# Kernel optimization log

Hardware: AMD Instinct MI355X
Metric: run time of the kernel (lower is better)

The kernel has to match this reference:

```python
import jax, jax.numpy as jnp
import numpy as np

N = 20000        # nodes
E = 320000       # edges (avg degree 16)
IN = 128         # in_channels
D = 64           # out_channels == per-head dim (PyG TransformerConv)
H = 4            # heads
EPS_BN = 1e-5


def setup_inputs() -> dict:
    key = jax.random.key(0)
    ks = jax.random.split(key, 12)
    x = jax.random.normal(ks[0], (N, IN), jnp.float32)
    edge_index = jax.random.randint(ks[1], (2, E), 0, N, dtype=jnp.int64)
    s = 1.0 / np.sqrt(IN)
    Wq = jax.random.normal(ks[2], (IN, H * D), jnp.float32) * s
    bq = jnp.zeros((H * D,), jnp.float32)
    Wk = jax.random.normal(ks[3], (IN, H * D), jnp.float32) * s
    bk = jnp.zeros((H * D,), jnp.float32)
    Wv = jax.random.normal(ks[4], (IN, H * D), jnp.float32) * s
    bv = jnp.zeros((H * D,), jnp.float32)
    Wskip = jax.random.normal(ks[5], (IN, D), jnp.float32) * s
    bskip = jnp.zeros((D,), jnp.float32)
    gamma = jnp.ones((D,), jnp.float32)
    beta = jnp.zeros((D,), jnp.float32)
    return {"x": x, "edge_index": edge_index, "Wq": Wq, "bq": bq,
            "Wk": Wk, "bk": bk, "Wv": Wv, "bv": bv,
            "Wskip": Wskip, "bskip": bskip, "gamma": gamma, "beta": beta}


def reference(x, edge_index, Wq, bq, Wk, bk, Wv, bv, Wskip, bskip, gamma, beta):
    src = edge_index[0]   # message source j
    dst = edge_index[1]   # message target i
    # node-level projections, [N, H, D]
    q = (x @ Wq + bq).reshape(N, H, D)
    k = (x @ Wk + bk).reshape(N, H, D)
    v = (x @ Wv + bv).reshape(N, H, D)
    # per-edge attention logits [E, H]
    scores = jnp.einsum('ehd,ehd->eh', q[dst], k[src]) / jnp.sqrt(jnp.float32(D))
    # segment softmax over incoming edges of each target node
    smax = jax.ops.segment_max(scores, dst, num_segments=N)
    smax = jnp.where(jnp.isfinite(smax), smax, 0.0)  # isolated nodes
    p = jnp.exp(scores - smax[dst])
    denom = jax.ops.segment_sum(p, dst, num_segments=N)
    alpha = p / (denom[dst] + 1e-16)                  # [E, H]
    # scatter-aggregate messages: [N, H, D]
    msg = jax.ops.segment_sum(alpha[:, :, None] * v[src], dst, num_segments=N)
    # concat=False -> mean over heads; root skip connection
    out = msg.mean(axis=1) + x @ Wskip + bskip        # [N, D]
    # BatchNorm1d over nodes (training-mode batch stats, biased var)
    mu = out.mean(axis=0)
    var = out.var(axis=0)
    out = (out - mu) * jax.lax.rsqrt(var + EPS_BN) * gamma + beta
    # exact (erf) GELU, dropout = identity at eval
    return jax.nn.gelu(out, approximate=False)
```

## Files before the change

### kernel.cpp

```cpp
#include <hip/hip_runtime.h>
#include <hip/hip_fp16.h>
#include <math.h>

#define NNODES 20000
#define NEDGES 320000
#define CIN 128
#define DOUT 64
#define NHEAD 4
#define HD 256
#define PROJW 320
#define KVW 512
#define NCOL 832
#define NWAVES (1250 * 13)

typedef __attribute__((ext_vector_type(8))) _Float16 half8;
typedef __attribute__((ext_vector_type(4))) float f32x4;

__global__ __launch_bounds__(256) void prep_kernel(
    const float* __restrict__ x,
    const float* __restrict__ Wq, const float* __restrict__ bq,
    const float* __restrict__ Wk, const float* __restrict__ bk,
    const float* __restrict__ Wv, const float* __restrict__ bv,
    const float* __restrict__ Ws, const float* __restrict__ bs,
    _Float16* __restrict__ xh, _Float16* __restrict__ Wth,
    float* __restrict__ bias832)
{
    int i = blockIdx.x * 256 + threadIdx.x;
    if (i < NNODES * CIN / 8) {
        const float4* xv = reinterpret_cast<const float4*>(x);
        float4 u = xv[2 * i], v = xv[2 * i + 1];
        half8 h = { (_Float16)u.x, (_Float16)u.y, (_Float16)u.z, (_Float16)u.w,
                    (_Float16)v.x, (_Float16)v.y, (_Float16)v.z, (_Float16)v.w };
        *reinterpret_cast<half8*>(xh + (size_t)i * 8) = h;
        return;
    }
    i -= NNODES * CIN / 8;
    if (i < NCOL * CIN) {
        int c = i >> 7, k = i & 127;
        float v;
        if (c < 256)      v = Wq[k * HD + c];
        else if (c < 512) v = Wk[k * HD + (c - 256)];
        else if (c < 768) v = Wv[k * HD + (c - 512)];
        else              v = Ws[k * DOUT + (c - 768)];
        Wth[(size_t)c * CIN + k] = (_Float16)v;
        return;
    }
    i -= NCOL * CIN;
    if (i < NCOL) {
        float v;
        if (i < 256)      v = bq[i];
        else if (i < 512) v = bk[i - 256];
        else if (i < 768) v = bv[i - 512];
        else              v = bs[i - 768];
        bias832[i] = v;
    }
}

__global__ __launch_bounds__(256) void wproj_kernel(
    const _Float16* __restrict__ xh, const _Float16* __restrict__ Wth,
    const float* __restrict__ bias832,
    float* __restrict__ proj, __half* __restrict__ kvh)
{
    const int wv = blockIdx.x * 4 + (threadIdx.x >> 6);
    if (wv >= NWAVES) return;
    const int l = threadIdx.x & 63;
    const int ct = wv / 1250, rt = wv % 1250;
    const int row0 = rt * 16, colb = ct * 64;
    const int lrow = l & 15, lk8 = (l >> 4) * 8;

    const _Float16* xr = xh + (size_t)(row0 + lrow) * CIN + lk8;
    const half8 a0 = *reinterpret_cast<const half8*>(xr);
    const half8 a1 = *reinterpret_cast<const half8*>(xr + 32);
    const half8 a2 = *reinterpret_cast<const half8*>(xr + 64);
    const half8 a3 = *reinterpret_cast<const half8*>(xr + 96);

    f32x4 acc[4];
    #pragma unroll
    for (int cg = 0; cg < 4; ++cg) {
        const _Float16* wr = Wth + (size_t)(colb + cg * 16 + lrow) * CIN + lk8;
        const half8 b0 = *reinterpret_cast<const half8*>(wr);
        const half8 b1 = *reinterpret_cast<const half8*>(wr + 32);
        const half8 b2 = *reinterpret_cast<const half8*>(wr + 64);
        const half8 b3 = *reinterpret_cast<const half8*>(wr + 96);
        f32x4 c = {0.f, 0.f, 0.f, 0.f};
        c = __builtin_amdgcn_mfma_f32_16x16x32_f16(a0, b0, c, 0, 0, 0);
        c = __builtin_amdgcn_mfma_f32_16x16x32_f16(a1, b1, c, 0, 0, 0);
        c = __builtin_amdgcn_mfma_f32_16x16x32_f16(a2, b2, c, 0, 0, 0);
        c = __builtin_amdgcn_mfma_f32_16x16x32_f16(a3, b3, c, 0, 0, 0);
        acc[cg] = c;
    }

    const int orow = row0 + (l >> 4) * 4;
    #pragma unroll
    for (int cg = 0; cg < 4; ++cg) {
        const int c = colb + cg * 16 + lrow;
        const float bias = bias832[c];
        if (ct < 4) {
            #pragma unroll
            for (int r = 0; r < 4; ++r)
                proj[(size_t)(orow + r) * PROJW + c] = acc[cg][r] + bias;
        } else if (ct < 12) {
            #pragma unroll
            for (int r = 0; r < 4; ++r)
                kvh[(size_t)(orow + r) * KVW + (c - 256)] = __float2half(acc[cg][r] + bias);
        } else {
            #pragma unroll
            for (int r = 0; r < 4; ++r)
                proj[(size_t)(orow + r) * PROJW + (c - 512)] = acc[cg][r] + bias;
        }
    }
}

__global__ void hist_kernel(const int* __restrict__ ei, int* __restrict__ deg)
{
    int e = blockIdx.x * blockDim.x + threadIdx.x;
    if (e >= NEDGES) return;
    atomicAdd(&deg[ei[NEDGES + e]], 1);
}

__global__ __launch_bounds__(1024) void scan_kernel(
    const int* __restrict__ deg, int* __restrict__ rowptr, int* __restrict__ cursor)
{
    __shared__ int sd[1024];
    const int t = threadIdx.x;
    const int chunk = 20;
    const int base = t * chunk;
    int tsum = 0;
    for (int i = 0; i < chunk; ++i) {
        int idx = base + i;
        tsum += (idx < NNODES) ? deg[idx] : 0;
    }
    sd[t] = tsum; __syncthreads();
    for (int off = 1; off < 1024; off <<= 1) {
        int v = (t >= off) ? sd[t - off] : 0;
        __syncthreads();
        sd[t] += v;
        __syncthreads();
    }
    int run = sd[t] - tsum;
    for (int i = 0; i < chunk; ++i) {
        int idx = base + i;
        if (idx < NNODES) {
            int d = deg[idx];
            rowptr[idx] = run; cursor[idx] = run;
            run += d;
        }
    }
    if (t == 1023) rowptr[NNODES] = sd[1023];
}

__global__ void scatter_kernel(const int* __restrict__ ei, int* __restrict__ cursor,
                               int* __restrict__ col)
{
    int e = blockIdx.x * blockDim.x + threadIdx.x;
    if (e >= NEDGES) return;
    int src = ei[e];
    int dst = ei[NEDGES + e];
    int pos = atomicAdd(&cursor[dst], 1);
    col[pos] = src;
}

__global__ __launch_bounds__(256) void attn_kernel(
    const float* __restrict__ proj, const __half* __restrict__ kvh,
    const int* __restrict__ rowptr, const int* __restrict__ col,
    float* __restrict__ out_pre)
{
    const int node = blockIdx.x * 4 + (threadIdx.x >> 6);
    if (node >= NNODES) return;
    const int lane = threadIdx.x & 63;
    const int lane4 = lane * 4;

    const float4 q = *reinterpret_cast<const float4*>(proj + (size_t)node * PROJW + lane4);

    float m = -INFINITY, l = 0.f;
    float ax = 0.f, ay = 0.f, az = 0.f, aw = 0.f;
    int p = rowptr[node];
    const int pend = rowptr[node + 1];

    int j = (p < pend) ? col[p] : 0;
    const __half* bj = kvh + (size_t)j * KVW + lane4;
    uint2 kraw = *reinterpret_cast<const uint2*>(bj);
    uint2 vraw = *reinterpret_cast<const uint2*>(bj + 256);

    for (; p < pend; ++p) {
        const int p1 = p + 1;
        const int jn = (p1 < pend) ? col[p1] : j;
        const __half* bn = kvh + (size_t)jn * KVW + lane4;
        const uint2 krawn = *reinterpret_cast<const uint2*>(bn);
        const uint2 vrawn = *reinterpret_cast<const uint2*>(bn + 256);

        const float2 k0 = __half22float2(*reinterpret_cast<const __half2*>(&kraw.x));
        const float2 k1 = __half22float2(*reinterpret_cast<const __half2*>(&kraw.y));
        float partial = q.x * k0.x + q.y * k0.y + q.z * k1.x + q.w * k1.y;
        partial += __shfl_xor(partial, 1, 16);
        partial += __shfl_xor(partial, 2, 16);
        partial += __shfl_xor(partial, 4, 16);
        partial += __shfl_xor(partial, 8, 16);
        const float s = partial * 0.125f;
        const float mnew = fmaxf(m, s);
        const float scale = __expf(m - mnew);
        const float pc = __expf(s - mnew);
        const float2 v0 = __half22float2(*reinterpret_cast<const __half2*>(&vraw.x));
        const float2 v1 = __half22float2(*reinterpret_cast<const __half2*>(&vraw.y));
        l = l * scale + pc;
        ax = ax * scale + pc * v0.x;
        ay = ay * scale + pc * v0.y;
        az = az * scale + pc * v1.x;
        aw = aw * scale + pc * v1.y;
        m = mnew;
        kraw = krawn; vraw = vrawn;
    }
    const float inv = 1.f / (l + 1e-16f);
    float rx = ax * inv, ry = ay * inv, rz = az * inv, rw = aw * inv;
    rx += __shfl_xor(rx, 16); rx += __shfl_xor(rx, 32);
    ry += __shfl_xor(ry, 16); ry += __shfl_xor(ry, 32);
    rz += __shfl_xor(rz, 16); rz += __shfl_xor(rz, 32);
    rw += __shfl_xor(rw, 16); rw += __shfl_xor(rw, 32);
    if (lane < 16) {
        const float4 sk = *reinterpret_cast<const float4*>(proj + (size_t)node * PROJW + 256 + lane4);
        float4 o;
        o.x = rx * 0.25f + sk.x;
        o.y = ry * 0.25f + sk.y;
        o.z = rz * 0.25f + sk.z;
        o.w = rw * 0.25f + sk.w;
        *reinterpret_cast<float4*>(out_pre + (size_t)node * DOUT + lane4) = o;
    }
}

__global__ __launch_bounds__(256) void bnred_kernel(
    const float* __restrict__ out_pre, float* __restrict__ bnacc)
{
    const int tid = threadIdx.x;
    const int c = tid & 63, g = tid >> 6;
    float s = 0.f, ss = 0.f;
    for (int r = blockIdx.x * 4 + g; r < NNODES; r += gridDim.x * 4) {
        float v = out_pre[(size_t)r * DOUT + c];
        s += v; ss += v * v;
    }
    __shared__ float sd[256];
    sd[tid] = s; __syncthreads();
    float s4 = 0.f;
    if (g == 0) s4 = sd[tid] + sd[tid + 64] + sd[tid + 128] + sd[tid + 192];
    __syncthreads();
    sd[tid] = ss; __syncthreads();
    if (g == 0) {
        float ss4 = sd[tid] + sd[tid + 64] + sd[tid + 128] + sd[tid + 192];
        atomicAdd(&bnacc[c], s4);
        atomicAdd(&bnacc[64 + c], ss4);
    }
}

__global__ __launch_bounds__(256) void final_kernel(
    const float* __restrict__ out_pre, const float* __restrict__ bnacc,
    const float* __restrict__ gamma, const float* __restrict__ beta,
    float* __restrict__ out)
{
    int idx = blockIdx.x * blockDim.x + threadIdx.x;
    if (idx >= NNODES * DOUT) return;
    const int c = idx & 63;
    const float mu = bnacc[c] * (1.f / NNODES);
    const float var = bnacc[64 + c] * (1.f / NNODES) - mu * mu;
    float v = (out_pre[idx] - mu) * rsqrtf(var + 1e-5f) * gamma[c] + beta[c];
    out[idx] = v * 0.5f * (1.f + erff(v * 0.70710678118654752f));
}

extern "C" void kernel_launch(void* const* d_in, const int* in_sizes, int n_in,
                              void* d_out, int out_size, void* d_ws, size_t ws_size,
                              hipStream_t stream) {
    const float* x     = (const float*)d_in[0];
    const int*   ei    = (const int*)d_in[1];
    const float* Wq    = (const float*)d_in[2];
    const float* bq    = (const float*)d_in[3];
    const float* Wk    = (const float*)d_in[4];
    const float* bk    = (const float*)d_in[5];
    const float* Wv    = (const float*)d_in[6];
    const float* bv    = (const float*)d_in[7];
    const float* Wskip = (const float*)d_in[8];
    const float* bskip = (const float*)d_in[9];
    const float* gamma = (const float*)d_in[10];
    const float* beta  = (const float*)d_in[11];
    float* out = (float*)d_out;

    __half*   kvh    = (__half*)d_ws;
    _Float16* xh     = (_Float16*)((char*)d_ws + 20480000);
    _Float16* Wth    = xh + (size_t)NNODES * CIN;
    float*    bias832= (float*)(Wth + (size_t)NCOL * CIN);
    float*    proj   = bias832 + NCOL;
    float*    out_pre= proj + (size_t)NNODES * PROJW;
    float*    bnacc  = out_pre + (size_t)NNODES * DOUT;
    int*      deg    = (int*)(bnacc + 128);
    int*      rowptr = deg + NNODES;
    int*      cursor = rowptr + NNODES + 1;
    int*      col    = cursor + NNODES;

    hipMemsetAsync(bnacc, 0, (128 + NNODES) * sizeof(int), stream);

    const int prep_total = NNODES * CIN / 8 + NCOL * CIN + NCOL;
    prep_kernel<<<(prep_total + 255) / 256, 256, 0, stream>>>(
        x, Wq, bq, Wk, bk, Wv, bv, Wskip, bskip, xh, Wth, bias832);
    wproj_kernel<<<(NWAVES + 3) / 4, 256, 0, stream>>>(xh, Wth, bias832, proj, kvh);
    hist_kernel<<<(NEDGES + 255) / 256, 256, 0, stream>>>(ei, deg);
    scan_kernel<<<1, 1024, 0, stream>>>(deg, rowptr, cursor);
    scatter_kernel<<<(NEDGES + 255) / 256, 256, 0, stream>>>(ei, cursor, col);
    attn_kernel<<<NNODES / 4, 256, 0, stream>>>(proj, kvh, rowptr, col, out_pre);
    bnred_kernel<<<128, 256, 0, stream>>>(out_pre, bnacc);
    final_kernel<<<(NNODES * DOUT + 255) / 256, 256, 0, stream>>>(
        out_pre, bnacc, gamma, beta, out);
}
```

Before: 264.6 us.

## Fuse graph build into projection kernels and BN reduction into attention

Merges the degree histogram into the prep kernel and the CSR scatter into the projection GEMM kernel as extra independent blocks. It also folds the BatchNorm sum and sum-of-squares reduction into the attention kernel, which now processes two nodes per wave and accumulates per-block partials before the atomics. This cuts the launch count from eight to five and removes the separate pass that re-read out_pre. In exchange it adds more global atomics on bnacc, one pair per block, and mixes heterogeneous work inside single launches.

```diff
diff --git a/kernel.cpp b/kernel.cpp
--- a/kernel.cpp
+++ b/kernel.cpp
@@ -12,18 +12,22 @@
 #define KVW 512
 #define NCOL 832
 #define NWAVES (1250 * 13)
+#define WPROJ_BLOCKS ((NWAVES + 3) / 4)
+#define SCATTER_BLOCKS ((NEDGES + 255) / 256)
+#define PREP_TOTAL (NNODES * CIN / 8 + NCOL * CIN + NCOL)
 
 typedef __attribute__((ext_vector_type(8))) _Float16 half8;
 typedef __attribute__((ext_vector_type(4))) float f32x4;
 
-__global__ __launch_bounds__(256) void prep_kernel(
+__global__ __launch_bounds__(256) void prep_hist_kernel(
     const float* __restrict__ x,
     const float* __restrict__ Wq, const float* __restrict__ bq,
     const float* __restrict__ Wk, const float* __restrict__ bk,
     const float* __restrict__ Wv, const float* __restrict__ bv,
     const float* __restrict__ Ws, const float* __restrict__ bs,
     _Float16* __restrict__ xh, _Float16* __restrict__ Wth,
-    float* __restrict__ bias832)
+    float* __restrict__ bias832,
+    const int* __restrict__ ei, int* __restrict__ deg)
 {
     int i = blockIdx.x * 256 + threadIdx.x;
     if (i < NNODES * CIN / 8) {
@@ -53,14 +57,60 @@
         else if (i < 768) v = bv[i - 512];
         else              v = bs[i - 768];
         bias832[i] = v;
-    }
-}
-
-__global__ __launch_bounds__(256) void wproj_kernel(
+        return;
+    }
+    i -= NCOL;
+    if (i < NEDGES)
+        atomicAdd(&deg[ei[NEDGES + i]], 1);
+}
+
+__global__ __launch_bounds__(1024) void scan_kernel(
+    const int* __restrict__ deg, int* __restrict__ rowptr, int* __restrict__ cursor)
+{
+    __shared__ int sd[1024];
+    const int t = threadIdx.x;
+    const int chunk = 20;
+    const int base = t * chunk;
+    int tsum = 0;
+    for (int i = 0; i < chunk; ++i) {
+        int idx = base + i;
+        tsum += (idx < NNODES) ? deg[idx] : 0;
+    }
+    sd[t] = tsum; __syncthreads();
+    for (int off = 1; off < 1024; off <<= 1) {
+        int v = (t >= off) ? sd[t - off] : 0;
+        __syncthreads();
+        sd[t] += v;
+        __syncthreads();
+    }
+    int run = sd[t] - tsum;
+    for (int i = 0; i < chunk; ++i) {
+        int idx = base + i;
+        if (idx < NNODES) {
+            int d = deg[idx];
+            rowptr[idx] = run; cursor[idx] = run;
+            run += d;
+        }
+    }
+    if (t == 1023) rowptr[NNODES] = sd[1023];
+}
+
+__global__ __launch_bounds__(256) void wproj_scatter_kernel(
     const _Float16* __restrict__ xh, const _Float16* __restrict__ Wth,
     const float* __restrict__ bias832,
-    float* __restrict__ proj, __half* __restrict__ kvh)
-{
+    float* __restrict__ proj, __half* __restrict__ kvh,
+    const int* __restrict__ ei, int* __restrict__ cursor, int* __restrict__ col)
+{
+    if (blockIdx.x >= WPROJ_BLOCKS) {
+        int e = (blockIdx.x - WPROJ_BLOCKS) * 256 + threadIdx.x;
+        if (e < NEDGES) {
+            int src = ei[e];
+            int dst = ei[NEDGES + e];
+            int pos = atomicAdd(&cursor[dst], 1);
+            col[pos] = src;
+        }
+        return;
+    }
     const int wv = blockIdx.x * 4 + (threadIdx.x >> 6);
     if (wv >= NWAVES) return;
     const int l = threadIdx.x & 63;
@@ -111,142 +161,94 @@
     }
 }
 
-__global__ void hist_kernel(const int* __restrict__ ei, int* __restrict__ deg)
-{
-    int e = blockIdx.x * blockDim.x + threadIdx.x;
-    if (e >= NEDGES) return;
-    atomicAdd(&deg[ei[NEDGES + e]], 1);
-}
-
-__global__ __launch_bounds__(1024) void scan_kernel(
-    const int* __restrict__ deg, int* __restrict__ rowptr, int* __restrict__ cursor)
-{
-    __shared__ int sd[1024];
-    const int t = threadIdx.x;
-    const int chunk = 20;
-    const int base = t * chunk;
-    int tsum = 0;
-    for (int i = 0; i < chunk; ++i) {
-        int idx = base + i;
-        tsum += (idx < NNODES) ? deg[idx] : 0;
-    }
-    sd[t] = tsum; __syncthreads();
-    for (int off = 1; off < 1024; off <<= 1) {
-        int v = (t >= off) ? sd[t - off] : 0;
-        __syncthreads();
-        sd[t] += v;
-        __syncthreads();
-    }
-    int run = sd[t] - tsum;
-    for (int i = 0; i < chunk; ++i) {
-        int idx = base + i;
-        if (idx < NNODES) {
-            int d = deg[idx];
-            rowptr[idx] = run; cursor[idx] = run;
-            run += d;
-        }
-    }
-    if (t == 1023) rowptr[NNODES] = sd[1023];
-}
-
-__global__ void scatter_kernel(const int* __restrict__ ei, int* __restrict__ cursor,
-                               int* __restrict__ col)
-{
-    int e = blockIdx.x * blockDim.x + threadIdx.x;
-    if (e >= NEDGES) return;
-    int src = ei[e];
-    int dst = ei[NEDGES + e];
-    int pos = atomicAdd(&cursor[dst], 1);
-    col[pos] = src;
-}
-
-__global__ __launch_bounds__(256) void attn_kernel(
+__global__ __launch_bounds__(256) void attn_bn_kernel(
     const float* __restrict__ proj, const __half* __restrict__ kvh,
     const int* __restrict__ rowptr, const int* __restrict__ col,
-    float* __restrict__ out_pre)
-{
-    const int node = blockIdx.x * 4 + (threadIdx.x >> 6);
-    if (node >= NNODES) return;
+    float* __restrict__ out_pre, float* __restrict__ bnacc)
+{
+    const int wave = threadIdx.x >> 6;
     const int lane = threadIdx.x & 63;
     const int lane4 = lane * 4;
-
-    const float4 q = *reinterpret_cast<const float4*>(proj + (size_t)node * PROJW + lane4);
-
-    float m = -INFINITY, l = 0.f;
-    float ax = 0.f, ay = 0.f, az = 0.f, aw = 0.f;
-    int p = rowptr[node];
-    const int pend = rowptr[node + 1];
-
-    int j = (p < pend) ? col[p] : 0;
-    const __half* bj = kvh + (size_t)j * KVW + lane4;
-    uint2 kraw = *reinterpret_cast<const uint2*>(bj);
-    uint2 vraw = *reinterpret_cast<const uint2*>(bj + 256);
-
-    for (; p < pend; ++p) {
-        const int p1 = p + 1;
-        const int jn = (p1 < pend) ? col[p1] : j;
-        const __half* bn = kvh + (size_t)jn * KVW + lane4;
-        const uint2 krawn = *reinterpret_cast<const uint2*>(bn);
-        const uint2 vrawn = *reinterpret_cast<const uint2*>(bn + 256);
-
-        const float2 k0 = __half22float2(*reinterpret_cast<const __half2*>(&kraw.x));
-        const float2 k1 = __half22float2(*reinterpret_cast<const __half2*>(&kraw.y));
-        float partial = q.x * k0.x + q.y * k0.y + q.z * k1.x + q.w * k1.y;
-        partial += __shfl_xor(partial, 1, 16);
-        partial += __shfl_xor(partial, 2, 16);
-        partial += __shfl_xor(partial, 4, 16);
-        partial += __shfl_xor(partial, 8, 16);
-        const float s = partial * 0.125f;
-        const float mnew = fmaxf(m, s);
-        const float scale = __expf(m - mnew);
-        const float pc = __expf(s - mnew);
-        const float2 v0 = __half22float2(*reinterpret_cast<const __half2*>(&vraw.x));
-        const float2 v1 = __half22float2(*reinterpret_cast<const __half2*>(&vraw.y));
-        l = l * scale + pc;
-        ax = ax * scale + pc * v0.x;
-        ay = ay * scale + pc * v0.y;
-        az = az * scale + pc * v1.x;
-        aw = aw * scale + pc * v1.y;
-        m = mnew;
-        kraw = krawn; vraw = vrawn;
-    }
-    const float inv = 1.f / (l + 1e-16f);
-    float rx = ax * inv, ry = ay * inv, rz = az * inv, rw = aw * inv;
-    rx += __shfl_xor(rx, 16); rx += __shfl_xor(rx, 32);
-    ry += __shfl_xor(ry, 16); ry += __shfl_xor(ry, 32);
-    rz += __shfl_xor(rz, 16); rz += __shfl_xor(rz, 32);
-    rw += __shfl_xor(rw, 16); rw += __shfl_xor(rw, 32);
+    float4 bsum  = make_float4(0.f, 0.f, 0.f, 0.f);
+    float4 bsum2 = make_float4(0.f, 0.f, 0.f, 0.f);
+
+    #pragma unroll
+    for (int t = 0; t < 2; ++t) {
+        const int node = blockIdx.x * 8 + wave * 2 + t;
+
+        const float4 q = *reinterpret_cast<const float4*>(proj + (size_t)node * PROJW + lane4);
+        float m = -INFINITY, l = 0.f;
+        float ax = 0.f, ay = 0.f, az = 0.f, aw = 0.f;
+        int p = rowptr[node];
+        const int pend = rowptr[node + 1];
+
+        int j = (p < pend) ? col[p] : 0;
+        const __half* bj = kvh + (size_t)j * KVW + lane4;
+        uint2 kraw = *reinterpret_cast<const uint2*>(bj);
+        uint2 vraw = *reinterpret_cast<const uint2*>(bj + 256);
+
+        for (; p < pend; ++p) {
+            const int p1 = p + 1;
+            const int jn = (p1 < pend) ? col[p1] : j;
+            const __half* bn = kvh + (size_t)jn * KVW + lane4;
+            const uint2 krawn = *reinterpret_cast<const uint2*>(bn);
+            const uint2 vrawn = *reinterpret_cast<const uint2*>(bn + 256);
+
+            const float2 k0 = __half22float2(*reinterpret_cast<const __half2*>(&kraw.x));
+            const float2 k1 = __half22float2(*reinterpret_cast<const __half2*>(&kraw.y));
+            float partial = q.x * k0.x + q.y * k0.y + q.z * k1.x + q.w * k1.y;
+            partial += __shfl_xor(partial, 1, 16);
+            partial += __shfl_xor(partial, 2, 16);
+            partial += __shfl_xor(partial, 4, 16);
+            partial += __shfl_xor(partial, 8, 16);
+            const float s = partial * 0.125f;
+            const float mnew = fmaxf(m, s);
+            const float scale = __expf(m - mnew);
+            const float pc = __expf(s - mnew);
+            const float2 v0 = __half22float2(*reinterpret_cast<const __half2*>(&vraw.x));
+            const float2 v1 = __half22float2(*reinterpret_cast<const __half2*>(&vraw.y));
+            l = l * scale + pc;
+            ax = ax * scale + pc * v0.x;
+            ay = ay * scale + pc * v0.y;
+            az = az * scale + pc * v1.x;
+            aw = aw * scale + pc * v1.y;
+            m = mnew;
+            kraw = krawn; vraw = vrawn;
+        }
+        const float inv = 1.f / (l + 1e-16f);
+        float rx = ax * inv, ry = ay * inv, rz = az * inv, rw = aw * inv;
+        rx += __shfl_xor(rx, 16); rx += __shfl_xor(rx, 32);
+        ry += __shfl_xor(ry, 16); ry += __shfl_xor(ry, 32);
+        rz += __shfl_xor(rz, 16); rz += __shfl_xor(rz, 32);
+        rw += __shfl_xor(rw, 16); rw += __shfl_xor(rw, 32);
+        if (lane < 16) {
+            const float4 sk = *reinterpret_cast<const float4*>(proj + (size_t)node * PROJW + 256 + lane4);
+            float4 o;
+            o.x = rx * 0.25f + sk.x;
+            o.y = ry * 0.25f + sk.y;
+            o.z = rz * 0.25f + sk.z;
+            o.w = rw * 0.25f + sk.w;
+            *reinterpret_cast<float4*>(out_pre + (size_t)node * DOUT + lane4) = o;
+            bsum.x += o.x; bsum.y += o.y; bsum.z += o.z; bsum.w += o.w;
+            bsum2.x += o.x * o.x; bsum2.y += o.y * o.y;
+            bsum2.z += o.z * o.z; bsum2.w += o.w * o.w;
+        }
+    }
+
+    __shared__ float sred[2][4][64];
     if (lane < 16) {
-        const float4 sk = *reinterpret_cast<const float4*>(proj + (size_t)node * PROJW + 256 + lane4);
-        float4 o;
-        o.x = rx * 0.25f + sk.x;
-        o.y = ry * 0.25f + sk.y;
-        o.z = rz * 0.25f + sk.z;
-        o.w = rw * 0.25f + sk.w;
-        *reinterpret_cast<float4*>(out_pre + (size_t)node * DOUT + lane4) = o;
-    }
-}
-
-__global__ __launch_bounds__(256) void bnred_kernel(
-    const float* __restrict__ out_pre, float* __restrict__ bnacc)
-{
-    const int tid = threadIdx.x;
-    const int c = tid & 63, g = tid >> 6;
-    float s = 0.f, ss = 0.f;
-    for (int r = blockIdx.x * 4 + g; r < NNODES; r += gridDim.x * 4) {
-        float v = out_pre[(size_t)r * DOUT + c];
-        s += v; ss += v * v;
-    }
-    __shared__ float sd[256];
-    sd[tid] = s; __syncthreads();
-    float s4 = 0.f;
-    if (g == 0) s4 = sd[tid] + sd[tid + 64] + sd[tid + 128] + sd[tid + 192];
+        sred[0][wave][lane4 + 0] = bsum.x;  sred[0][wave][lane4 + 1] = bsum.y;
+        sred[0][wave][lane4 + 2] = bsum.z;  sred[0][wave][lane4 + 3] = bsum.w;
+        sred[1][wave][lane4 + 0] = bsum2.x; sred[1][wave][lane4 + 1] = bsum2.y;
+        sred[1][wave][lane4 + 2] = bsum2.z; sred[1][wave][lane4 + 3] = bsum2.w;
+    }
     __syncthreads();
-    sd[tid] = ss; __syncthreads();
-    if (g == 0) {
-        float ss4 = sd[tid] + sd[tid + 64] + sd[tid + 128] + sd[tid + 192];
-        atomicAdd(&bnacc[c], s4);
-        atomicAdd(&bnacc[64 + c], ss4);
+    if (threadIdx.x < 64) {
+        const int c = threadIdx.x;
+        float s  = sred[0][0][c] + sred[0][1][c] + sred[0][2][c] + sred[0][3][c];
+        float ss = sred[1][0][c] + sred[1][1][c] + sred[1][2][c] + sred[1][3][c];
+        atomicAdd(&bnacc[c], s);
+        atomicAdd(&bnacc[64 + c], ss);
     }
 }
 
@@ -295,15 +297,13 @@
 
     hipMemsetAsync(bnacc, 0, (128 + NNODES) * sizeof(int), stream);
 
-    const int prep_total = NNODES * CIN / 8 + NCOL * CIN + NCOL;
-    prep_kernel<<<(prep_total + 255) / 256, 256, 0, stream>>>(
-        x, Wq, bq, Wk, bk, Wv, bv, Wskip, bskip, xh, Wth, bias832);
-    wproj_kernel<<<(NWAVES + 3) / 4, 256, 0, stream>>>(xh, Wth, bias832, proj, kvh);
-    hist_kernel<<<(NEDGES + 255) / 256, 256, 0, stream>>>(ei, deg);
+    const int ph_total = PREP_TOTAL + NEDGES;
+    prep_hist_kernel<<<(ph_total + 255) / 256, 256, 0, stream>>>(
+        x, Wq, bq, Wk, bk, Wv, bv, Wskip, bskip, xh, Wth, bias832, ei, deg);
     scan_kernel<<<1, 1024, 0, stream>>>(deg, rowptr, cursor);
-    scatter_kernel<<<(NEDGES + 255) / 256, 256, 0, stream>>>(ei, cursor, col);
-    attn_kernel<<<NNODES / 4, 256, 0, stream>>>(proj, kvh, rowptr, col, out_pre);
-    bnred_kernel<<<128, 256, 0, stream>>>(out_pre, bnacc);
+    wproj_scatter_kernel<<<WPROJ_BLOCKS + SCATTER_BLOCKS, 256, 0, stream>>>(
+        xh, Wth, bias832, proj, kvh, ei, cursor, col);
+    attn_bn_kernel<<<NNODES / 8, 256, 0, stream>>>(proj, kvh, rowptr, col, out_pre, bnacc);
     final_kernel<<<(NNODES * DOUT + 255) / 256, 256, 0, stream>>>(
         out_pre, bnacc, gamma, beta, out);
 }
```

Result: slower. 299.4 us (+13.1%).
